# Optimization experiments

Hardware: AMD Instinct MI355X
Metric: run time of the kernel (lower is better)

## Reference

```python
import jax, jax.numpy as jnp
import numpy as np

B, F, DIN, HID, H, E, NC = 2048, 32, 64, 128, 4, 262144, 10
N = B * F  # 65536 nodes


def setup_inputs() -> dict:
    key = jax.random.key(0)
    ks = jax.random.split(key, 20)
    p = lambda k, shape: jax.random.normal(k, shape, jnp.float32) * 0.05
    return {
        "emb": jax.random.normal(ks[0], (B, F, DIN), jnp.float32),
        "edge_index": jax.random.randint(ks[1], (2, E), 0, N, jnp.int32),
        "batch": (jnp.arange(N, dtype=jnp.int32) // F),
        # aligner Linear(64 -> 128)
        "W_align": p(ks[2], (DIN, HID)), "b_align": p(ks[3], (HID,)),
        # GATConv1: 128 -> 128, heads=4, concat
        "W1": p(ks[4], (HID, H * HID)),
        "att_src1": p(ks[5], (H, HID)), "att_dst1": p(ks[6], (H, HID)),
        "b1": p(ks[7], (H * HID,)),
        # GATConv2: 512 -> 128, heads=1, concat=False
        "W2": p(ks[8], (H * HID, HID)),
        "att_src2": p(ks[9], (1, HID)), "att_dst2": p(ks[10], (1, HID)),
        "b2": p(ks[11], (HID,)),
        # classifier MLP 128 -> 64 -> 10
        "Wc1": p(ks[12], (HID, HID // 2)), "bc1": p(ks[13], (HID // 2,)),
        "Wc2": p(ks[14], (HID // 2, NC)), "bc2": p(ks[15], (NC,)),
    }


def _gat(x, src, dst, W, a_src, a_dst, b, concat):
    # PyG GATConv (eval mode): per-edge additive attention + segment softmax over dst.
    n = x.shape[0]
    h, c = a_src.shape
    hx = (x @ W).reshape(n, h, c)                       # [N,H,C]
    al_s = jnp.einsum('nhc,hc->nh', hx, a_src)          # [N,H]
    al_d = jnp.einsum('nhc,hc->nh', hx, a_dst)
    e = jax.nn.leaky_relu(al_s[src] + al_d[dst], 0.2)   # [E,H]
    m = jax.ops.segment_max(e, dst, num_segments=n)
    m = jnp.where(jnp.isfinite(m), m, 0.0)
    ex = jnp.exp(e - m[dst])
    denom = jax.ops.segment_sum(ex, dst, num_segments=n)
    alpha = ex / (denom[dst] + 1e-16)                   # [E,H]
    out = jax.ops.segment_sum(alpha[:, :, None] * hx[src], dst, num_segments=n)
    out = out.reshape(n, h * c) if concat else out.mean(axis=1)
    return out + b


def reference(emb, edge_index, batch, W_align, b_align, W1, att_src1, att_dst1, b1,
              W2, att_src2, att_dst2, b2, Wc1, bc1, Wc2, bc2):
    # fused align: Linear over stacked field embeddings, then flatten to nodes
    x = (emb @ W_align + b_align).reshape(N, HID)
    # add self-loops (PyG GATConv default)
    loop = jnp.arange(N, dtype=edge_index.dtype)
    src = jnp.concatenate([edge_index[0], loop])
    dst = jnp.concatenate([edge_index[1], loop])
    x = _gat(x, src, dst, W1, att_src1, att_dst1, b1, concat=True)
    x = jax.nn.elu(x)
    x = _gat(x, src, dst, W2, att_src2, att_dst2, b2, concat=False)
    # global mean pool per graph
    g = jax.ops.segment_sum(x, batch, num_segments=B)
    cnt = jax.ops.segment_sum(jnp.ones((N, 1), x.dtype), batch, num_segments=B)
    g = g / jnp.maximum(cnt, 1.0)
    # classifier head (dropout off in eval)
    hcls = jax.nn.leaky_relu(g @ Wc1 + bc1, 0.01)
    return hcls @ Wc2 + bc2
```

## Files before the change

### kernel.cpp

```cpp
#include <hip/hip_runtime.h>


namespace {

constexpr int NNODE = 65536;
constexpr int NEDGE = 262144;
constexpr int NGRAPH = 2048;
constexpr int FPG = 32;

typedef __attribute__((ext_vector_type(8))) short bf16x8;
typedef __attribute__((ext_vector_type(4))) float f32x4;

__device__ __forceinline__ float lrelu02(float x) { return x > 0.f ? x : 0.2f * x; }
__device__ __forceinline__ float bf_lo(unsigned u) { return __uint_as_float(u << 16); }
__device__ __forceinline__ float bf_hi(unsigned u) { return __uint_as_float(u & 0xffff0000u); }
__device__ __forceinline__ float b2f(unsigned short u) { return __uint_as_float(((unsigned)u) << 16); }
__device__ __forceinline__ unsigned short f2b(float f) {
  unsigned u = __float_as_uint(f);
  return (unsigned short)((u + 0x7fffu + ((u >> 16) & 1u)) >> 16);
}

__device__ __forceinline__ void gload16(const void* g, unsigned short* l) {
  __builtin_amdgcn_global_load_lds((const __attribute__((address_space(1))) void*)g,
                                   (__attribute__((address_space(3))) void*)l, 16, 0, 0);
}


__global__ __launch_bounds__(256) void prep_kernel(const float* __restrict__ W1, const float* __restrict__ W2,
                                                   const float* __restrict__ Wa, const float* __restrict__ as1,
                                                   const float* __restrict__ ad1, unsigned short* __restrict__ w1t,
                                                   unsigned short* __restrict__ w2t, unsigned short* __restrict__ wat,
                                                   float* __restrict__ vs1, float* __restrict__ vd1,
                                                   int* __restrict__ deg) {
  int b = blockIdx.x;
  int tid = threadIdx.x;
  if (b < 256) {
    int idx = b * 256 + tid;
    int n = idx >> 7, k = idx & 127;
    w1t[idx] = f2b(W1[(size_t)k * 512 + n]);
  } else if (b < 512) {
    int idx = (b - 256) * 256 + tid;
    int n = idx >> 9, k = idx & 511;
    w2t[idx] = f2b(W2[(size_t)k * 128 + n]);
  } else if (b < 544) {
    int idx = (b - 512) * 256 + tid;
    int n = idx >> 6, k = idx & 63;
    wat[idx] = f2b(Wa[(size_t)k * 128 + n]);
  } else if (b < 546) {
    int idx = (b - 544) * 256 + tid;
    int h = idx >> 7, c = idx & 127;
    float s = 0.f, d = 0.f;
    const float* wrow = W1 + (size_t)c * 512 + h * 128;
    const float* ar = as1 + h * 128;
    const float* dr = ad1 + h * 128;
    for (int j = 0; j < 128; ++j) {
      float w = wrow[j];
      s += w * ar[j];
      d += w * dr[j];
    }
    vs1[idx] = s;
    vd1[idx] = d;
  } else {
    int idx = (b - 546) * 256 + tid;
    int4 z;
    z.x = 0; z.y = 0; z.z = 0; z.w = 0;
    *(int4*)&deg[idx * 4] = z;
  }
}


__global__ __launch_bounds__(256) void hist_kernel(const int* __restrict__ dst, int* __restrict__ deg) {
  int e = blockIdx.x * 256 + threadIdx.x;
  if (e < NEDGE) atomicAdd(&deg[dst[e]], 1);
}

__global__ __launch_bounds__(1024) void scan_kernel(const int* __restrict__ deg, int* __restrict__ rowptr,
                                                    int* __restrict__ cursor) {
  __shared__ int sums[1024];
  int t = threadIdx.x;
  int base = t * 64;
  int d[64];
  int s = 0;
#pragma unroll
  for (int i = 0; i < 16; ++i) {
    int4 v = *(const int4*)&deg[base + i * 4];
    d[4 * i] = v.x; d[4 * i + 1] = v.y; d[4 * i + 2] = v.z; d[4 * i + 3] = v.w;
    s += v.x + v.y + v.z + v.w;
  }
  sums[t] = s;
  __syncthreads();
  for (int off = 1; off < 1024; off <<= 1) {
    int v = (t >= off) ? sums[t - off] : 0;
    __syncthreads();
    sums[t] += v;
    __syncthreads();
  }
  int run = (t == 0) ? 0 : sums[t - 1];
#pragma unroll
  for (int i = 0; i < 16; ++i) {
    int4 r;
    r.x = run; run += d[4 * i];
    r.y = run; run += d[4 * i + 1];
    r.z = run; run += d[4 * i + 2];
    r.w = run; run += d[4 * i + 3];
    *(int4*)&rowptr[base + i * 4] = r;
    *(int4*)&cursor[base + i * 4] = r;
  }
  if (t == 1023) rowptr[NNODE] = run;
}

__global__ __launch_bounds__(256) void scatter_kernel(const int* __restrict__ src, const int* __restrict__ dst,
                                                      int* __restrict__ cursor, int* __restrict__ csr_src,
                                                      int* __restrict__ csr_dst) {
  int e = blockIdx.x * 256 + threadIdx.x;
  if (e < NEDGE) {
    int s = src[e], d = dst[e];
    int p = atomicAdd(&cursor[d], 1);
    csr_src[p] = s;
    csr_dst[p] = d;
  }
}


__global__ __launch_bounds__(256) void edgew1_kernel(const int* __restrict__ csr_src, const int* __restrict__ csr_dst,
                                                     const float* __restrict__ al_s, const float* __restrict__ al_d,
                                                     float* __restrict__ w1) {
  int p = blockIdx.x * 256 + threadIdx.x;
  if (p >= NEDGE) return;
  int s = csr_src[p], d = csr_dst[p];
  float4 as = *(const float4*)&al_s[s * 4];
  float4 ad = *(const float4*)&al_d[d * 4];
  float4 w;
  w.x = expf(lrelu02(as.x + ad.x));
  w.y = expf(lrelu02(as.y + ad.y));
  w.z = expf(lrelu02(as.z + ad.z));
  w.w = expf(lrelu02(as.w + ad.w));
  *(float4*)&w1[(size_t)p * 4] = w;
}

__global__ __launch_bounds__(256) void edgew2_kernel(const int* __restrict__ csr_src, const int* __restrict__ csr_dst,
                                                     const float* __restrict__ al_s, const float* __restrict__ al_d,
                                                     float* __restrict__ w2) {
  int p = blockIdx.x * 256 + threadIdx.x;
  if (p >= NEDGE) return;
  w2[p] = expf(lrelu02(al_s[csr_src[p]] + al_d[csr_dst[p]]));
}


__device__ __forceinline__ bf16x8 frag_ld(const unsigned short* lds, int row, int kbyte) {
  const char* base = (const char*)lds + row * 128;
  int sw = (row & 7) << 4;
  uint2 lo = *(const uint2*)(base + (kbyte ^ sw));
  uint2 hi = *(const uint2*)(base + ((kbyte + 32) ^ sw));
  union { bf16x8 v; uint2 u2[2]; } f;
  f.u2[0] = lo;
  f.u2[1] = hi;
  return f.v;
}

__device__ __forceinline__ bf16x8 frag_ld_x(const unsigned short* lds, int row, int kbyte) {
  const char* base = (const char*)lds + row * 256;
  int sw = (row & 7) << 4;
  uint2 lo = *(const uint2*)(base + (kbyte ^ sw));
  uint2 hi = *(const uint2*)(base + ((kbyte + 32) ^ sw));
  union { bf16x8 v; uint2 u2[2]; } f;
  f.u2[0] = lo;
  f.u2[1] = hi;
  return f.v;
}


__global__ __launch_bounds__(256) void align_mfma_kernel(const float* __restrict__ emb,
                                                         const unsigned short* __restrict__ wat,
                                                         const float* __restrict__ bias,
                                                         unsigned short* __restrict__ x0) {
  __shared__ char smem[36864];
  unsigned short* Ae = (unsigned short*)smem;
  unsigned short* Wt = (unsigned short*)(smem + 16384);
  const int tid = threadIdx.x;
  const int lane = tid & 63;
  const int w = tid >> 6;
  const size_t bm = (size_t)blockIdx.x * 128;
  const int ln = lane & 15, lg = lane >> 4;
  const int kb0 = lg << 3;

  {
    int r8 = lane >> 3;
    int b8 = (lane & 7) << 4;
#pragma unroll
    for (int i = 0; i < 4; ++i) {
      int row = w * 32 + i * 8 + r8;
      int bcol = b8 ^ ((row & 7) << 4);
      gload16((const char*)wat + row * 128 + bcol, Wt + w * 2048 + i * 512);
    }
  }
#pragma unroll
  for (int i = 0; i < 4; ++i) {
    int slot = i * 256 + tid;
    int row = slot >> 3;
    int c16 = slot & 7;
    const float* sp = emb + (bm + row) * 64 + c16 * 8;
    float4 a = *(const float4*)sp;
    float4 b = *(const float4*)(sp + 4);
    ushort4 o0, o1;
    o0.x = f2b(a.x); o0.y = f2b(a.y); o0.z = f2b(a.z); o0.w = f2b(a.w);
    o1.x = f2b(b.x); o1.y = f2b(b.y); o1.z = f2b(b.z); o1.w = f2b(b.w);
    char* dp = (char*)Ae + row * 128 + ((c16 * 16) ^ ((row & 7) << 4));
    *(ushort4*)dp = o0;
    *(ushort4*)(dp + 8) = o1;
  }
  __syncthreads();

  f32x4 zero = {0.f, 0.f, 0.f, 0.f};
  f32x4 acc[2][8];
#pragma unroll
  for (int i = 0; i < 2; ++i)
#pragma unroll
    for (int j = 0; j < 8; ++j) acc[i][j] = zero;

#pragma unroll
  for (int kw = 0; kw < 2; ++kw) {
    bf16x8 af0 = frag_ld(Ae, w * 32 + ln, kw * 64 + kb0);
    bf16x8 af1 = frag_ld(Ae, w * 32 + 16 + ln, kw * 64 + kb0);
#pragma unroll
    for (int nf = 0; nf < 8; ++nf) {
      bf16x8 bfr = frag_ld(Wt, nf * 16 + ln, kw * 64 + kb0);
      acc[0][nf] = __builtin_amdgcn_mfma_f32_16x16x32_bf16(af0, bfr, acc[0][nf], 0, 0, 0);
      acc[1][nf] = __builtin_amdgcn_mfma_f32_16x16x32_bf16(af1, bfr, acc[1][nf], 0, 0, 0);
    }
  }

  float bval[8];
#pragma unroll
  for (int nf = 0; nf < 8; ++nf) bval[nf] = bias[nf * 16 + ln];
  __syncthreads();
  unsigned short* Cs = (unsigned short*)smem;
#pragma unroll
  for (int mf = 0; mf < 2; ++mf) {
#pragma unroll
    for (int r = 0; r < 4; ++r) {
      unsigned short* rp = Cs + (w * 32 + mf * 16 + lg * 4 + r) * 136 + ln;
#pragma unroll
      for (int nf = 0; nf < 8; ++nf) rp[nf * 16] = f2b(acc[mf][nf][r] + bval[nf]);
    }
  }
  __syncthreads();
  const int r16 = tid >> 4;
  const int cchunk = (tid & 15) * 8;
#pragma unroll
  for (int it = 0; it < 8; ++it) {
    int row = it * 16 + r16;
    *(uint4*)(x0 + (bm + row) * 128 + cchunk) = *(const uint4*)(Cs + row * 136 + cchunk);
  }
}


__global__ __launch_bounds__(256, 2) void fused12_kernel(const unsigned short* __restrict__ ybar,
                                                         const unsigned short* __restrict__ w1t,
                                                         const unsigned short* __restrict__ w2t,
                                                         const float* __restrict__ b1,
                                                         const float* __restrict__ as2,
                                                         const float* __restrict__ ad2,
                                                         unsigned short* __restrict__ hx2,
                                                         float* __restrict__ al_s2, float* __restrict__ al_d2) {
  __shared__ char smem[65536];
  unsigned short* Ws = (unsigned short*)smem;
  unsigned short* Ys = Ws + 16384;

  const int tid = threadIdx.x;
  const int lane = tid & 63;
  const int w = tid >> 6;
  const size_t bm = (size_t)blockIdx.x * 128;

  const int ln = lane & 15, lg = lane >> 4;
  const int kb0 = lg << 3;
  const int drow = lane >> 4;
  const int dcol = (lane & 15) << 4;

  f32x4 zero = {0.f, 0.f, 0.f, 0.f};
  f32x4 acc2[2][8];
#pragma unroll
  for (int i = 0; i < 2; ++i)
#pragma unroll
    for (int j = 0; j < 8; ++j) acc2[i][j] = zero;

  for (int h = 0; h < 4; ++h) {
    if (h) __syncthreads();
#pragma unroll
    for (int i = 0; i < 8; ++i) {
      int row = w * 32 + i * 4 + drow;
      int bcol = dcol ^ ((row & 7) << 4);
      gload16((const char*)w1t + ((size_t)(h * 128 + row) << 8) + bcol, Ws + w * 4096 + i * 512);
      gload16((const char*)ybar + ((bm + row) << 10) + (h << 8) + bcol, Ys + w * 4096 + i * 512);
    }
    __syncthreads();

    f32x4 acc1[8][2];
#pragma unroll
    for (int i = 0; i < 8; ++i) {
      acc1[i][0] = zero;
      acc1[i][1] = zero;
    }
#pragma unroll
    for (int kw = 0; kw < 4; ++kw) {
      bf16x8 bfr0 = frag_ld_x(Ys, w * 32 + ln, kw * 64 + kb0);
      bf16x8 bfr1 = frag_ld_x(Ys, w * 32 + 16 + ln, kw * 64 + kb0);
#pragma unroll
      for (int ct = 0; ct < 8; ++ct) {
        bf16x8 af = frag_ld_x(Ws, ct * 16 + ln, kw * 64 + kb0);
        acc1[ct][0] = __builtin_amdgcn_mfma_f32_16x16x32_bf16(af, bfr0, acc1[ct][0], 0, 0, 0);
        acc1[ct][1] = __builtin_amdgcn_mfma_f32_16x16x32_bf16(af, bfr1, acc1[ct][1], 0, 0, 0);
      }
    }
    __syncthreads();

#pragma unroll
    for (int i = 0; i < 8; ++i) {
      int row = w * 32 + i * 4 + drow;
      int bcol = dcol ^ ((row & 7) << 4);
      gload16((const char*)w2t + ((size_t)row << 10) + (h << 8) + bcol, Ws + w * 4096 + i * 512);
    }
    __syncthreads();

#pragma unroll
    for (int kw = 0; kw < 4; ++kw) {
      float4 b_lo = *(const float4*)&b1[h * 128 + kw * 32 + lg * 4];
      float4 b_hi = *(const float4*)&b1[h * 128 + kw * 32 + 16 + lg * 4];
      bf16x8 af2[2];
#pragma unroll
      for (int mf = 0; mf < 2; ++mf) {
        union { bf16x8 v; unsigned short u[8]; } t;
#pragma unroll
        for (int r = 0; r < 4; ++r) {
          float vlo = acc1[2 * kw][mf][r] + ((const float*)&b_lo)[r];
          float vhi = acc1[2 * kw + 1][mf][r] + ((const float*)&b_hi)[r];
          vlo = vlo > 0.f ? vlo : __expf(vlo) - 1.f;
          vhi = vhi > 0.f ? vhi : __expf(vhi) - 1.f;
          t.u[r] = f2b(vlo);
          t.u[4 + r] = f2b(vhi);
        }
        af2[mf] = t.v;
      }
#pragma unroll
      for (int nf = 0; nf < 8; ++nf) {
        bf16x8 bfr = frag_ld_x(Ws, nf * 16 + ln, kw * 64 + kb0);
        acc2[0][nf] = __builtin_amdgcn_mfma_f32_16x16x32_bf16(af2[0], bfr, acc2[0][nf], 0, 0, 0);
        acc2[1][nf] = __builtin_amdgcn_mfma_f32_16x16x32_bf16(af2[1], bfr, acc2[1][nf], 0, 0, 0);
      }
    }
  }

  __syncthreads();
  unsigned short* Cs = (unsigned short*)smem;
#pragma unroll
  for (int mf = 0; mf < 2; ++mf) {
#pragma unroll
    for (int r = 0; r < 4; ++r) {
      unsigned short* rp = Cs + (w * 32 + mf * 16 + lg * 4 + r) * 136 + ln;
#pragma unroll
      for (int nf = 0; nf < 8; ++nf) rp[nf * 16] = f2b(acc2[mf][nf][r]);
    }
  }
  __syncthreads();
  if (tid < 128) {
    const unsigned short* row = Cs + tid * 136;
    float s = 0.f, d = 0.f;
#pragma unroll 4
    for (int c = 0; c < 128; ++c) {
      float v = b2f(row[c]);
      s += v * as2[c];
      d += v * ad2[c];
    }
    al_s2[bm + tid] = s;
    al_d2[bm + tid] = d;
  }
  const int r16 = tid >> 4;
  const int cchunk = (tid & 15) * 8;
#pragma unroll
  for (int it = 0; it < 8; ++it) {
    int row = it * 16 + r16;
    *(uint4*)(hx2 + (bm + row) * 128 + cchunk) = *(const uint4*)(Cs + row * 136 + cchunk);
  }
}


__global__ __launch_bounds__(256) void al1_kernel(const unsigned short* __restrict__ x0,
                                                  const float* __restrict__ vs1, const float* __restrict__ vd1,
                                                  float* __restrict__ al_s, float* __restrict__ al_d) {
  int n = blockIdx.x * 4 + (threadIdx.x >> 6);
  int lane = threadIdx.x & 63;
  unsigned v = *(const unsigned*)&x0[(size_t)n * 128 + lane * 2];
  float v0 = bf_lo(v), v1 = bf_hi(v);
  float r[8];
#pragma unroll
  for (int h = 0; h < 4; ++h) {
    float2 as = *(const float2*)&vs1[h * 128 + lane * 2];
    float2 ad = *(const float2*)&vd1[h * 128 + lane * 2];
    r[h] = v0 * as.x + v1 * as.y;
    r[4 + h] = v0 * ad.x + v1 * ad.y;
  }
#pragma unroll
  for (int off = 32; off; off >>= 1) {
#pragma unroll
    for (int j = 0; j < 8; ++j) r[j] += __shfl_xor(r[j], off);
  }
  if (lane < 4)
    al_s[n * 4 + lane] = r[lane];
  else if (lane < 8)
    al_d[n * 4 + lane - 4] = r[lane];
}


__global__ __launch_bounds__(256) void agg1_kernel(const unsigned short* __restrict__ x0,
                                                   const float* __restrict__ al_s, const float* __restrict__ al_d,
                                                   const int* __restrict__ rowptr, const int* __restrict__ csr_src,
                                                   const float* __restrict__ w1, unsigned short* __restrict__ ybar) {
  int n = blockIdx.x * 4 + (threadIdx.x >> 6);
  int c2 = (threadIdx.x & 63) * 2;
  float4 As4 = *(const float4*)&al_s[n * 4];
  float4 Ad4 = *(const float4*)&al_d[n * 4];
  float w00 = expf(lrelu02(As4.x + Ad4.x));
  float w01 = expf(lrelu02(As4.y + Ad4.y));
  float w02 = expf(lrelu02(As4.z + Ad4.z));
  float w03 = expf(lrelu02(As4.w + Ad4.w));
  unsigned u = *(const unsigned*)&x0[(size_t)n * 128 + c2];
  float lo = bf_lo(u), hi = bf_hi(u);
  float a00 = w00 * lo, a01 = w01 * lo, a02 = w02 * lo, a03 = w03 * lo;
  float a10 = w00 * hi, a11 = w01 * hi, a12 = w02 * hi, a13 = w03 * hi;
  float d0 = w00, d1 = w01, d2 = w02, d3 = w03;
  int p0 = rowptr[n], p1 = rowptr[n + 1];
  int p = p0;
  for (; p + 4 <= p1; p += 4) {
    int s0 = csr_src[p], s1 = csr_src[p + 1], s2 = csr_src[p + 2], s3 = csr_src[p + 3];
    float4 wA = *(const float4*)&w1[(size_t)p * 4];
    float4 wB = *(const float4*)&w1[(size_t)(p + 1) * 4];
    float4 wC = *(const float4*)&w1[(size_t)(p + 2) * 4];
    float4 wD = *(const float4*)&w1[(size_t)(p + 3) * 4];
    unsigned u0 = *(const unsigned*)&x0[(size_t)s0 * 128 + c2];
    unsigned u1 = *(const unsigned*)&x0[(size_t)s1 * 128 + c2];
    unsigned u2 = *(const unsigned*)&x0[(size_t)s2 * 128 + c2];
    unsigned u3 = *(const unsigned*)&x0[(size_t)s3 * 128 + c2];
    float l0 = bf_lo(u0), h0 = bf_hi(u0);
    float l1 = bf_lo(u1), h1 = bf_hi(u1);
    float l2 = bf_lo(u2), h2 = bf_hi(u2);
    float l3 = bf_lo(u3), h3 = bf_hi(u3);
    a00 += wA.x * l0 + wB.x * l1 + wC.x * l2 + wD.x * l3;
    a01 += wA.y * l0 + wB.y * l1 + wC.y * l2 + wD.y * l3;
    a02 += wA.z * l0 + wB.z * l1 + wC.z * l2 + wD.z * l3;
    a03 += wA.w * l0 + wB.w * l1 + wC.w * l2 + wD.w * l3;
    a10 += wA.x * h0 + wB.x * h1 + wC.x * h2 + wD.x * h3;
    a11 += wA.y * h0 + wB.y * h1 + wC.y * h2 + wD.y * h3;
    a12 += wA.z * h0 + wB.z * h1 + wC.z * h2 + wD.z * h3;
    a13 += wA.w * h0 + wB.w * h1 + wC.w * h2 + wD.w * h3;
    d0 += wA.x + wB.x + wC.x + wD.x;
    d1 += wA.y + wB.y + wC.y + wD.y;
    d2 += wA.z + wB.z + wC.z + wD.z;
    d3 += wA.w + wB.w + wC.w + wD.w;
  }
  for (; p < p1; ++p) {
    int s = csr_src[p];
    float4 wA = *(const float4*)&w1[(size_t)p * 4];
    unsigned uu = *(const unsigned*)&x0[(size_t)s * 128 + c2];
    float l = bf_lo(uu), hh = bf_hi(uu);
    a00 += wA.x * l; a01 += wA.y * l; a02 += wA.z * l; a03 += wA.w * l;
    a10 += wA.x * hh; a11 += wA.y * hh; a12 += wA.z * hh; a13 += wA.w * hh;
    d0 += wA.x; d1 += wA.y; d2 += wA.z; d3 += wA.w;
  }
  unsigned short* yb = ybar + (size_t)n * 512 + c2;
  float i0 = 1.f / (d0 + 1e-16f), i1 = 1.f / (d1 + 1e-16f);
  float i2 = 1.f / (d2 + 1e-16f), i3 = 1.f / (d3 + 1e-16f);
  ushort2 o;
  o.x = f2b(a00 * i0); o.y = f2b(a10 * i0); *(ushort2*)(yb + 0) = o;
  o.x = f2b(a01 * i1); o.y = f2b(a11 * i1); *(ushort2*)(yb + 128) = o;
  o.x = f2b(a02 * i2); o.y = f2b(a12 * i2); *(ushort2*)(yb + 256) = o;
  o.x = f2b(a03 * i3); o.y = f2b(a13 * i3); *(ushort2*)(yb + 384) = o;
}


__global__ __launch_bounds__(256) void agg2_kernel(const unsigned short* __restrict__ hx,
                                                   const float* __restrict__ al_s, const float* __restrict__ al_d,
                                                   const int* __restrict__ rowptr, const int* __restrict__ csr_src,
                                                   const float* __restrict__ w2, const float* __restrict__ b2,
                                                   unsigned short* __restrict__ out) {
  int n = blockIdx.x * 4 + (threadIdx.x >> 6);
  int c2 = (threadIdx.x & 63) * 2;
  float w0 = expf(lrelu02(al_s[n] + al_d[n]));
  unsigned u = *(const unsigned*)&hx[(size_t)n * 128 + c2];
  float acc0 = w0 * bf_lo(u), acc1 = w0 * bf_hi(u);
  float den = w0;
  int p0 = rowptr[n], p1 = rowptr[n + 1];
  int p = p0;
  for (; p + 4 <= p1; p += 4) {
    int s0 = csr_src[p], s1 = csr_src[p + 1], s2 = csr_src[p + 2], s3 = csr_src[p + 3];
    float wa = w2[p], wb = w2[p + 1], wc = w2[p + 2], wd = w2[p + 3];
    unsigned u0 = *(const unsigned*)&hx[(size_t)s0 * 128 + c2];
    unsigned u1 = *(const unsigned*)&hx[(size_t)s1 * 128 + c2];
    unsigned u2 = *(const unsigned*)&hx[(size_t)s2 * 128 + c2];
    unsigned u3 = *(const unsigned*)&hx[(size_t)s3 * 128 + c2];
    acc0 += wa * bf_lo(u0) + wb * bf_lo(u1) + wc * bf_lo(u2) + wd * bf_lo(u3);
    acc1 += wa * bf_hi(u0) + wb * bf_hi(u1) + wc * bf_hi(u2) + wd * bf_hi(u3);
    den += wa + wb + wc + wd;
  }
  for (; p < p1; ++p) {
    int s = csr_src[p];
    float w = w2[p];
    unsigned uu = *(const unsigned*)&hx[(size_t)s * 128 + c2];
    acc0 += w * bf_lo(uu);
    acc1 += w * bf_hi(uu);
    den += w;
  }
  float inv = 1.f / (den + 1e-16f);
  ushort2 o;
  o.x = f2b(acc0 * inv + b2[c2]);
  o.y = f2b(acc1 * inv + b2[c2 + 1]);
  *(ushort2*)&out[(size_t)n * 128 + c2] = o;
}


__global__ __launch_bounds__(128) void poolcls_kernel(const unsigned short* __restrict__ x,
                                                      const float* __restrict__ Wc1, const float* __restrict__ bc1,
                                                      const float* __restrict__ Wc2, const float* __restrict__ bc2,
                                                      float* __restrict__ out) {
  __shared__ float g[128];
  __shared__ float hcls[64];
  int b = blockIdx.x;
  int t = threadIdx.x;
  const unsigned short* base = x + (size_t)b * FPG * 128;
  float s = 0.f;
#pragma unroll
  for (int i = 0; i < FPG; ++i) s += b2f(base[i * 128 + t]);
  g[t] = s * (1.0f / FPG);
  __syncthreads();
  if (t < 64) {
    float a = bc1[t];
#pragma unroll 4
    for (int k = 0; k < 128; ++k) a += g[k] * Wc1[k * 64 + t];
    hcls[t] = a > 0.f ? a : 0.01f * a;
  }
  __syncthreads();
  if (t < 10) {
    float a = bc2[t];
#pragma unroll
    for (int k = 0; k < 64; ++k) a += hcls[k] * Wc2[k * 10 + t];
    out[b * 10 + t] = a;
  }
}

}

extern "C" void kernel_launch(void* const* d_in, const int* in_sizes, int n_in,
                              void* d_out, int out_size, void* d_ws, size_t ws_size,
                              hipStream_t stream) {
  const float* emb = (const float*)d_in[0];
  const int* edge = (const int*)d_in[1];
  const float* W_align = (const float*)d_in[3];
  const float* b_align = (const float*)d_in[4];
  const float* W1 = (const float*)d_in[5];
  const float* att_src1 = (const float*)d_in[6];
  const float* att_dst1 = (const float*)d_in[7];
  const float* b1 = (const float*)d_in[8];
  const float* W2 = (const float*)d_in[9];
  const float* att_src2 = (const float*)d_in[10];
  const float* att_dst2 = (const float*)d_in[11];
  const float* b2 = (const float*)d_in[12];
  const float* Wc1 = (const float*)d_in[13];
  const float* bc1 = (const float*)d_in[14];
  const float* Wc2 = (const float*)d_in[15];
  const float* bc2 = (const float*)d_in[16];

  char* ws = (char*)d_ws;
  size_t off = 0;
  auto alloc = [&](size_t bytes) -> char* {
    char* p = ws + off;
    off += (bytes + 255) & ~(size_t)255;
    return p;
  };
  unsigned short* x0 = (unsigned short*)alloc((size_t)NNODE * 128 * 2);
  unsigned short* ybar = (unsigned short*)alloc((size_t)NNODE * 512 * 2);
  unsigned short* hx2 = (unsigned short*)alloc((size_t)NNODE * 128 * 2);
  unsigned short* out2 = (unsigned short*)alloc((size_t)NNODE * 128 * 2);
  float* al_s1 = (float*)alloc((size_t)NNODE * 4 * 4);
  float* al_d1 = (float*)alloc((size_t)NNODE * 4 * 4);
  float* al_s2 = (float*)alloc((size_t)NNODE * 4);
  float* al_d2 = (float*)alloc((size_t)NNODE * 4);
  int* deg = (int*)alloc((size_t)NNODE * 4);
  int* rowptr = (int*)alloc((size_t)(NNODE + 1) * 4);
  int* cursor = (int*)alloc((size_t)NNODE * 4);
  int* csr_src = (int*)alloc((size_t)NEDGE * 4);
  int* csr_dst = (int*)alloc((size_t)NEDGE * 4);
  float* w1 = (float*)alloc((size_t)NEDGE * 4 * 4);
  float* w2 = (float*)alloc((size_t)NEDGE * 4);
  unsigned short* w1t = (unsigned short*)alloc((size_t)512 * 128 * 2);
  unsigned short* w2t = (unsigned short*)alloc((size_t)128 * 512 * 2);
  unsigned short* wat = (unsigned short*)alloc((size_t)128 * 64 * 2);
  float* vs1 = (float*)alloc((size_t)512 * 4);
  float* vd1 = (float*)alloc((size_t)512 * 4);

  const int* src = edge;
  const int* dst = edge + NEDGE;

  prep_kernel<<<610, 256, 0, stream>>>(W1, W2, W_align, att_src1, att_dst1,
                                       w1t, w2t, wat, vs1, vd1, deg);
  hist_kernel<<<NEDGE / 256, 256, 0, stream>>>(dst, deg);
  scan_kernel<<<1, 1024, 0, stream>>>(deg, rowptr, cursor);
  scatter_kernel<<<NEDGE / 256, 256, 0, stream>>>(src, dst, cursor, csr_src, csr_dst);

  align_mfma_kernel<<<512, 256, 0, stream>>>(emb, wat, b_align, x0);
  al1_kernel<<<NNODE / 4, 256, 0, stream>>>(x0, vs1, vd1, al_s1, al_d1);
  edgew1_kernel<<<NEDGE / 256, 256, 0, stream>>>(csr_src, csr_dst, al_s1, al_d1, w1);
  agg1_kernel<<<NNODE / 4, 256, 0, stream>>>(x0, al_s1, al_d1, rowptr, csr_src, w1, ybar);
  fused12_kernel<<<512, 256, 0, stream>>>(ybar, w1t, w2t, b1, att_src2, att_dst2, hx2, al_s2, al_d2);
  edgew2_kernel<<<NEDGE / 256, 256, 0, stream>>>(csr_src, csr_dst, al_s2, al_d2, w2);
  agg2_kernel<<<NNODE / 4, 256, 0, stream>>>(hx2, al_s2, al_d2, rowptr, csr_src, w2, b2, out2);
  poolcls_kernel<<<NGRAPH, 128, 0, stream>>>(out2, Wc1, bc1, Wc2, bc2, (float*)d_out);
}
```

Before: 227.0 us.

## Fuse attention logits into align GEMM and agg2 into pooling classifier

The layer-1 attention logit computation (al1 kernel) moves into the align MFMA epilogue, using fp32 accumulators reduced with shuffles, so x0 is no longer re-read. agg2 and the pool/classifier are merged into one per-graph kernel that sums aggregated rows in registers and shared memory, which drops the out2 buffer write and re-read and removes two launches. The trade-off is that agg2 now runs only 2048 blocks, each walking 8 nodes per wave serially, so latency hiding drops. The logits are also now taken from fp32 values rather than bf16-rounded ones, which changes the numerics slightly.

```diff
diff --git a/kernel.cpp b/kernel.cpp
--- a/kernel.cpp
+++ b/kernel.cpp
@@ -173,7 +173,10 @@
 __global__ __launch_bounds__(256) void align_mfma_kernel(const float* __restrict__ emb,
                                                          const unsigned short* __restrict__ wat,
                                                          const float* __restrict__ bias,
-                                                         unsigned short* __restrict__ x0) {
+                                                         const float* __restrict__ vs1,
+                                                         const float* __restrict__ vd1,
+                                                         unsigned short* __restrict__ x0,
+                                                         float* __restrict__ al_s, float* __restrict__ al_d) {
   __shared__ char smem[36864];
   unsigned short* Ae = (unsigned short*)smem;
   unsigned short* Wt = (unsigned short*)(smem + 16384);
@@ -233,6 +236,40 @@
   float bval[8];
 #pragma unroll
   for (int nf = 0; nf < 8; ++nf) bval[nf] = bias[nf * 16 + ln];
+
+#pragma unroll
+  for (int h = 0; h < 4; ++h) {
+    float vsv[8], vdv[8];
+#pragma unroll
+    for (int nf = 0; nf < 8; ++nf) {
+      vsv[nf] = vs1[h * 128 + nf * 16 + ln];
+      vdv[nf] = vd1[h * 128 + nf * 16 + ln];
+    }
+#pragma unroll
+    for (int mf = 0; mf < 2; ++mf) {
+#pragma unroll
+      for (int r = 0; r < 4; ++r) {
+        float s = 0.f, d = 0.f;
+#pragma unroll
+        for (int nf = 0; nf < 8; ++nf) {
+          float v = acc[mf][nf][r] + bval[nf];
+          s += v * vsv[nf];
+          d += v * vdv[nf];
+        }
+#pragma unroll
+        for (int off = 1; off < 16; off <<= 1) {
+          s += __shfl_xor(s, off);
+          d += __shfl_xor(d, off);
+        }
+        if (ln == 0) {
+          size_t row = bm + w * 32 + mf * 16 + lg * 4 + r;
+          al_s[row * 4 + h] = s;
+          al_d[row * 4 + h] = d;
+        }
+      }
+    }
+  }
+
   __syncthreads();
   unsigned short* Cs = (unsigned short*)smem;
 #pragma unroll
@@ -381,33 +418,6 @@
     int row = it * 16 + r16;
     *(uint4*)(hx2 + (bm + row) * 128 + cchunk) = *(const uint4*)(Cs + row * 136 + cchunk);
   }
-}
-
-
-__global__ __launch_bounds__(256) void al1_kernel(const unsigned short* __restrict__ x0,
-                                                  const float* __restrict__ vs1, const float* __restrict__ vd1,
-                                                  float* __restrict__ al_s, float* __restrict__ al_d) {
-  int n = blockIdx.x * 4 + (threadIdx.x >> 6);
-  int lane = threadIdx.x & 63;
-  unsigned v = *(const unsigned*)&x0[(size_t)n * 128 + lane * 2];
-  float v0 = bf_lo(v), v1 = bf_hi(v);
-  float r[8];
-#pragma unroll
-  for (int h = 0; h < 4; ++h) {
-    float2 as = *(const float2*)&vs1[h * 128 + lane * 2];
-    float2 ad = *(const float2*)&vd1[h * 128 + lane * 2];
-    r[h] = v0 * as.x + v1 * as.y;
-    r[4 + h] = v0 * ad.x + v1 * ad.y;
-  }
-#pragma unroll
-  for (int off = 32; off; off >>= 1) {
-#pragma unroll
-    for (int j = 0; j < 8; ++j) r[j] += __shfl_xor(r[j], off);
-  }
-  if (lane < 4)
-    al_s[n * 4 + lane] = r[lane];
-  else if (lane < 8)
-    al_d[n * 4 + lane - 4] = r[lane];
 }
 
 
@@ -477,72 +487,73 @@
 }
 
 
-__global__ __launch_bounds__(256) void agg2_kernel(const unsigned short* __restrict__ hx,
-                                                   const float* __restrict__ al_s, const float* __restrict__ al_d,
-                                                   const int* __restrict__ rowptr, const int* __restrict__ csr_src,
-                                                   const float* __restrict__ w2, const float* __restrict__ b2,
-                                                   unsigned short* __restrict__ out) {
-  int n = blockIdx.x * 4 + (threadIdx.x >> 6);
-  int c2 = (threadIdx.x & 63) * 2;
-  float w0 = expf(lrelu02(al_s[n] + al_d[n]));
-  unsigned u = *(const unsigned*)&hx[(size_t)n * 128 + c2];
-  float acc0 = w0 * bf_lo(u), acc1 = w0 * bf_hi(u);
-  float den = w0;
-  int p0 = rowptr[n], p1 = rowptr[n + 1];
-  int p = p0;
-  for (; p + 4 <= p1; p += 4) {
-    int s0 = csr_src[p], s1 = csr_src[p + 1], s2 = csr_src[p + 2], s3 = csr_src[p + 3];
-    float wa = w2[p], wb = w2[p + 1], wc = w2[p + 2], wd = w2[p + 3];
-    unsigned u0 = *(const unsigned*)&hx[(size_t)s0 * 128 + c2];
-    unsigned u1 = *(const unsigned*)&hx[(size_t)s1 * 128 + c2];
-    unsigned u2 = *(const unsigned*)&hx[(size_t)s2 * 128 + c2];
-    unsigned u3 = *(const unsigned*)&hx[(size_t)s3 * 128 + c2];
-    acc0 += wa * bf_lo(u0) + wb * bf_lo(u1) + wc * bf_lo(u2) + wd * bf_lo(u3);
-    acc1 += wa * bf_hi(u0) + wb * bf_hi(u1) + wc * bf_hi(u2) + wd * bf_hi(u3);
-    den += wa + wb + wc + wd;
-  }
-  for (; p < p1; ++p) {
-    int s = csr_src[p];
-    float w = w2[p];
-    unsigned uu = *(const unsigned*)&hx[(size_t)s * 128 + c2];
-    acc0 += w * bf_lo(uu);
-    acc1 += w * bf_hi(uu);
-    den += w;
-  }
-  float inv = 1.f / (den + 1e-16f);
-  ushort2 o;
-  o.x = f2b(acc0 * inv + b2[c2]);
-  o.y = f2b(acc1 * inv + b2[c2 + 1]);
-  *(ushort2*)&out[(size_t)n * 128 + c2] = o;
-}
-
-
-__global__ __launch_bounds__(128) void poolcls_kernel(const unsigned short* __restrict__ x,
-                                                      const float* __restrict__ Wc1, const float* __restrict__ bc1,
-                                                      const float* __restrict__ Wc2, const float* __restrict__ bc2,
-                                                      float* __restrict__ out) {
+__global__ __launch_bounds__(256) void agg2pool_kernel(const unsigned short* __restrict__ hx,
+                                                       const float* __restrict__ al_s, const float* __restrict__ al_d,
+                                                       const int* __restrict__ rowptr, const int* __restrict__ csr_src,
+                                                       const float* __restrict__ w2, const float* __restrict__ b2,
+                                                       const float* __restrict__ Wc1, const float* __restrict__ bc1,
+                                                       const float* __restrict__ Wc2, const float* __restrict__ bc2,
+                                                       float* __restrict__ out) {
+  __shared__ float gsum[4][128];
   __shared__ float g[128];
   __shared__ float hcls[64];
-  int b = blockIdx.x;
-  int t = threadIdx.x;
-  const unsigned short* base = x + (size_t)b * FPG * 128;
-  float s = 0.f;
-#pragma unroll
-  for (int i = 0; i < FPG; ++i) s += b2f(base[i * 128 + t]);
-  g[t] = s * (1.0f / FPG);
-  __syncthreads();
-  if (t < 64) {
-    float a = bc1[t];
+  const int bgraph = blockIdx.x;
+  const int tid = threadIdx.x;
+  const int w4 = tid >> 6;
+  const int c2 = (tid & 63) * 2;
+
+  float ps0 = 0.f, ps1 = 0.f;
+#pragma unroll
+  for (int it = 0; it < 8; ++it) {
+    int n = bgraph * FPG + it * 4 + w4;
+    float w0 = expf(lrelu02(al_s[n] + al_d[n]));
+    unsigned u = *(const unsigned*)&hx[(size_t)n * 128 + c2];
+    float acc0 = w0 * bf_lo(u), acc1 = w0 * bf_hi(u);
+    float den = w0;
+    int p0 = rowptr[n], p1 = rowptr[n + 1];
+    int p = p0;
+    for (; p + 4 <= p1; p += 4) {
+      int s0 = csr_src[p], s1 = csr_src[p + 1], s2 = csr_src[p + 2], s3 = csr_src[p + 3];
+      float wa = w2[p], wb = w2[p + 1], wc = w2[p + 2], wd = w2[p + 3];
+      unsigned u0 = *(const unsigned*)&hx[(size_t)s0 * 128 + c2];
+      unsigned u1 = *(const unsigned*)&hx[(size_t)s1 * 128 + c2];
+      unsigned u2 = *(const unsigned*)&hx[(size_t)s2 * 128 + c2];
+      unsigned u3 = *(const unsigned*)&hx[(size_t)s3 * 128 + c2];
+      acc0 += wa * bf_lo(u0) + wb * bf_lo(u1) + wc * bf_lo(u2) + wd * bf_lo(u3);
+      acc1 += wa * bf_hi(u0) + wb * bf_hi(u1) + wc * bf_hi(u2) + wd * bf_hi(u3);
+      den += wa + wb + wc + wd;
+    }
+    for (; p < p1; ++p) {
+      int s = csr_src[p];
+      float w = w2[p];
+      unsigned uu = *(const unsigned*)&hx[(size_t)s * 128 + c2];
+      acc0 += w * bf_lo(uu);
+      acc1 += w * bf_hi(uu);
+      den += w;
+    }
+    float inv = 1.f / (den + 1e-16f);
+    ps0 += acc0 * inv;
+    ps1 += acc1 * inv;
+  }
+  gsum[w4][c2] = ps0;
+  gsum[w4][c2 + 1] = ps1;
+  __syncthreads();
+  if (tid < 128) {
+    g[tid] = (gsum[0][tid] + gsum[1][tid] + gsum[2][tid] + gsum[3][tid]) * (1.0f / FPG) + b2[tid];
+  }
+  __syncthreads();
+  if (tid < 64) {
+    float a = bc1[tid];
 #pragma unroll 4
-    for (int k = 0; k < 128; ++k) a += g[k] * Wc1[k * 64 + t];
-    hcls[t] = a > 0.f ? a : 0.01f * a;
-  }
-  __syncthreads();
-  if (t < 10) {
-    float a = bc2[t];
-#pragma unroll
-    for (int k = 0; k < 64; ++k) a += hcls[k] * Wc2[k * 10 + t];
-    out[b * 10 + t] = a;
+    for (int k = 0; k < 128; ++k) a += g[k] * Wc1[k * 64 + tid];
+    hcls[tid] = a > 0.f ? a : 0.01f * a;
+  }
+  __syncthreads();
+  if (tid < 10) {
+    float a = bc2[tid];
+#pragma unroll
+    for (int k = 0; k < 64; ++k) a += hcls[k] * Wc2[k * 10 + tid];
+    out[bgraph * 10 + tid] = a;
   }
 }
 
@@ -578,7 +589,6 @@
   unsigned short* x0 = (unsigned short*)alloc((size_t)NNODE * 128 * 2);
   unsigned short* ybar = (unsigned short*)alloc((size_t)NNODE * 512 * 2);
   unsigned short* hx2 = (unsigned short*)alloc((size_t)NNODE * 128 * 2);
-  unsigned short* out2 = (unsigned short*)alloc((size_t)NNODE * 128 * 2);
   float* al_s1 = (float*)alloc((size_t)NNODE * 4 * 4);
   float* al_d1 = (float*)alloc((size_t)NNODE * 4 * 4);
   float* al_s2 = (float*)alloc((size_t)NNODE * 4);
@@ -605,12 +615,11 @@
   scan_kernel<<<1, 1024, 0, stream>>>(deg, rowptr, cursor);
   scatter_kernel<<<NEDGE / 256, 256, 0, stream>>>(src, dst, cursor, csr_src, csr_dst);
 
-  align_mfma_kernel<<<512, 256, 0, stream>>>(emb, wat, b_align, x0);
-  al1_kernel<<<NNODE / 4, 256, 0, stream>>>(x0, vs1, vd1, al_s1, al_d1);
+  align_mfma_kernel<<<512, 256, 0, stream>>>(emb, wat, b_align, vs1, vd1, x0, al_s1, al_d1);
   edgew1_kernel<<<NEDGE / 256, 256, 0, stream>>>(csr_src, csr_dst, al_s1, al_d1, w1);
   agg1_kernel<<<NNODE / 4, 256, 0, stream>>>(x0, al_s1, al_d1, rowptr, csr_src, w1, ybar);
   fused12_kernel<<<512, 256, 0, stream>>>(ybar, w1t, w2t, b1, att_src2, att_dst2, hx2, al_s2, al_d2);
   edgew2_kernel<<<NEDGE / 256, 256, 0, stream>>>(csr_src, csr_dst, al_s2, al_d2, w2);
-  agg2_kernel<<<NNODE / 4, 256, 0, stream>>>(hx2, al_s2, al_d2, rowptr, csr_src, w2, b2, out2);
-  poolcls_kernel<<<NGRAPH, 128, 0, stream>>>(out2, Wc1, bc1, Wc2, bc2, (float*)d_out);
-}
+  agg2pool_kernel<<<NGRAPH, 256, 0, stream>>>(hx2, al_s2, al_d2, rowptr, csr_src, w2, b2,
+                                              Wc1, bc1, Wc2, bc2, (float*)d_out);
+}
```

After: 204.8 us. 9.8% less time.
